# Kernel tuning notes

Measured on AMD Instinct MI355X. Metric: run time of the kernel, lower is better.

## Reference

```python
import jax, jax.numpy as jnp
import numpy as np

DILATION = 1  # module init dilation


def _pd_indexing1d(x, d, dilation):
    # x: (B, C, T) float; d: (B, 1, T) float pitch-dependent dilation factors
    B, C, T = x.shape
    dil = jnp.clip((d * dilation).astype(jnp.int32), 1)          # (B,1,T), min 1
    idx = jnp.arange(T, dtype=jnp.int32)[None, None, :]          # (1,1,T)
    idxP = jnp.abs(idx - dil) % T                                # past indices
    idxF0 = idx + dil
    # torch sets overflowed idx to -(idx % T) - 1, i.e. wraps to T - 1 - (idx % T)
    idxF = jnp.where(idxF0 >= T, T - 1 - (idxF0 % T), idxF0)     # future indices
    xP = jnp.take_along_axis(x, jnp.broadcast_to(idxP, x.shape), axis=2)
    xF = jnp.take_along_axis(x, jnp.broadcast_to(idxF, x.shape), axis=2)
    return xP, x, xF


def setup_inputs() -> dict:
    key = jax.random.key(0)
    k1, k2, k3, k4, k5, k6 = jax.random.split(key, 6)
    B, Cin, Cout, T = 8, 512, 512, 8192
    x = jax.random.normal(k1, (B, Cin, T), dtype=jnp.float32)
    d = jax.random.uniform(k2, (B, 1, T), dtype=jnp.float32)
    s = 1.0 / np.sqrt(Cin)
    W0 = jax.random.uniform(k3, (Cout, Cin), jnp.float32, -s, s)  # conv with bias
    b0 = jax.random.uniform(k4, (Cout,), jnp.float32, -s, s)
    W1 = jax.random.uniform(k5, (Cout, Cin), jnp.float32, -s, s)  # no bias
    W2 = jax.random.uniform(k6, (Cout, Cin), jnp.float32, -s, s)  # no bias
    return {"x": x, "d": d, "W0": W0, "b0": b0, "W1": W1, "W2": W2}


def reference(x, d, W0, b0, W1, W2):
    xP, xC, xF = _pd_indexing1d(x, d, DILATION)
    # three 1x1 convs (channel-mixing matmuls), summed; bias only on first conv
    out = jnp.einsum('oc,bct->bot', W0, xP) + b0[None, :, None]
    out = out + jnp.einsum('oc,bct->bot', W1, xC)
    out = out + jnp.einsum('oc,bct->bot', W2, xF)
    return out
```

## Files before the change

kernel.cpp:

```cpp
#include <hip/hip_runtime.h>

#define TT 8192
#define CIN 512
#define COUT 512
#define NB 8
#define KTOT 1536
#define NT 24

typedef __attribute__((ext_vector_type(4))) float f32x4;
typedef __attribute__((ext_vector_type(8))) short bf16x8;
typedef __attribute__((ext_vector_type(8))) unsigned short u16x8;

#define GLD16(g, l) __builtin_amdgcn_global_load_lds(                      \
    (const __attribute__((address_space(1))) void*)(g),                    \
    (__attribute__((address_space(3))) void*)(l), 16, 0, 0)

#define CFENCE() asm volatile("" ::: "memory")
#define SBAR() do { CFENCE(); __builtin_amdgcn_s_barrier(); CFENCE(); } while (0)
#define VMCNT6() asm volatile("s_waitcnt vmcnt(6)" ::: "memory")
#define VMCNT2() asm volatile("s_waitcnt vmcnt(2)" ::: "memory")
#define VMCNT0() asm volatile("s_waitcnt vmcnt(0)" ::: "memory")
#define LGKM0() asm volatile("s_waitcnt lgkmcnt(0)" ::: "memory")
#define MFMA(a_, b_, c_) __builtin_amdgcn_mfma_f32_16x16x32_bf16((a_), (b_), (c_), 0, 0, 0)

__device__ inline unsigned short f2bf(float f) {
  union { float f; unsigned int u; } v; v.f = f;
  unsigned int u = v.u;
  unsigned int r = (u + 0x7FFFu + ((u >> 16) & 1u)) >> 16;
  return (unsigned short)r;
}

__global__ void k_convert_w(const float* __restrict__ W0, const float* __restrict__ W1,
                            const float* __restrict__ W2, unsigned short* __restrict__ Wb) {
  int i = blockIdx.x * 256 + threadIdx.x;
  if (i >= COUT * CIN) return;
  const float* Ws = blockIdx.y == 0 ? W0 : (blockIdx.y == 1 ? W1 : W2);
  int o = i >> 9, c = i & 511;
  Wb[(size_t)o * KTOT + blockIdx.y * CIN + c] = f2bf(Ws[i]);
}

__global__ void k_transpose(const float* __restrict__ x, unsigned short* __restrict__ xbT,
                            int b_base) {
  int b = b_base + blockIdx.z;
  const float* xb = x + (size_t)b * CIN * TT;
  unsigned short* xo = xbT + (size_t)blockIdx.z * TT * CIN;
  __shared__ float tile[64][65];
  int t0 = blockIdx.x * 64, c0 = blockIdx.y * 64;
  int tid = threadIdx.x;
#pragma unroll
  for (int it = 0; it < 16; ++it) {
    int L = it * 256 + tid;
    int c = L >> 6, t = L & 63;
    tile[c][t] = xb[(size_t)(c0 + c) * TT + (t0 + t)];
  }
  __syncthreads();
#pragma unroll
  for (int it = 0; it < 16; ++it) {
    int L = it * 256 + tid;
    int t = L >> 6, c = L & 63;
    xo[(size_t)(t0 + t) * CIN + (c0 + c)] = f2bf(tile[c][t]);
  }
}

__global__ __launch_bounds__(512) void k_gemm256(
    const unsigned short* __restrict__ Wb, const unsigned short* __restrict__ xbT,
    const float* __restrict__ d, const float* __restrict__ bias,
    float* __restrict__ out) {
  __shared__ __align__(16) unsigned short As[2][256 * 64];
  __shared__ __align__(16) unsigned short Bs[2][256 * 64];
  const int b = blockIdx.x;
  const int t0 = (blockIdx.y >> 1) * 256;
  const int row0 = (blockIdx.y & 1) * 256;
  const unsigned short* xb = xbT + (size_t)b * TT * CIN;
  const int tid = threadIdx.x;
  const int lane = tid & 63, wid = tid >> 6;
  const int wr = wid >> 2, wc = wid & 3;
  const int l15 = lane & 15, kg = lane >> 4;

  const int srow = tid >> 3;
  const int cSrc8 = (((tid & 7) ^ ((tid >> 4) & 7))) * 8;
  int aOff[4];
  int bOff[3][4];
#pragma unroll
  for (int j = 0; j < 4; ++j) {
    int r = j * 64 + srow;
    aOff[j] = (row0 + r) * KTOT + cSrc8;
    int t = t0 + r;
    float dv = d[(size_t)b * TT + t];
    int dil = (int)dv; if (dil < 1) dil = 1;
    int p = t - dil; if (p < 0) p = -p; p &= (TT - 1);
    int f0 = t + dil;
    int f = (f0 >= TT) ? (TT - 1 - (f0 & (TT - 1))) : f0;
    bOff[0][j] = p * CIN + cSrc8;
    bOff[1][j] = t * CIN + cSrc8;
    bOff[2][j] = f * CIN + cSrc8;
  }

  const int s7 = l15 >> 1;
  const int chunk0 = (kg ^ (s7 & 3)) + (s7 & 4);
  const int dK = (l15 & 8) ? -32 : 32;
  int aRd[2][4], bRd[2][2];
#pragma unroll
  for (int mh = 0; mh < 2; ++mh)
#pragma unroll
    for (int mi = 0; mi < 4; ++mi)
      aRd[mh][mi] = (wr * 128 + mh * 64 + mi * 16 + l15) * 64 + chunk0 * 8;
#pragma unroll
  for (int nh = 0; nh < 2; ++nh)
#pragma unroll
    for (int ni = 0; ni < 2; ++ni)
      bRd[nh][ni] = (wc * 64 + nh * 32 + ni * 16 + l15) * 64 + chunk0 * 8;

#define STAGE_A_G0(tc_, buf_) do {                                            \
    GLD16(Wb + aOff[0] + (tc_) * 64, &As[buf_][0 * 4096 + wid * 512]);        \
    GLD16(Wb + aOff[2] + (tc_) * 64, &As[buf_][2 * 4096 + wid * 512]);        \
  } while (0)
#define STAGE_A_G1(tc_, buf_) do {                                            \
    GLD16(Wb + aOff[1] + (tc_) * 64, &As[buf_][1 * 4096 + wid * 512]);        \
    GLD16(Wb + aOff[3] + (tc_) * 64, &As[buf_][3 * 4096 + wid * 512]);        \
  } while (0)
#define STAGE_B4(tc_, buf_) do {                                              \
    _Pragma("unroll") for (int j = 0; j < 4; ++j)                             \
      GLD16(xb + bOff[(tc_) >> 3][j] + ((tc_) & 7) * 64,                      \
            &Bs[buf_][j * 4096 + wid * 512]);                                 \
  } while (0)

  STAGE_B4(0, 0); STAGE_A_G0(0, 0); STAGE_A_G1(0, 0);
  VMCNT0();
  SBAR();

  bf16x8 af[4][2], bf0[2][2], bf1[2][2];
  f32x4 acc[8][4] = {};

#pragma unroll 2
  for (int tc = 0; tc < NT; ++tc) {
    const int cur = tc & 1;
#pragma unroll
    for (int mi = 0; mi < 4; ++mi) {
      af[mi][0] = *(const bf16x8*)&As[cur][aRd[0][mi]];
      af[mi][1] = *(const bf16x8*)&As[cur][aRd[0][mi] + dK];
    }
#pragma unroll
    for (int ni = 0; ni < 2; ++ni) {
      bf0[ni][0] = *(const bf16x8*)&Bs[cur][bRd[0][ni]];
      bf0[ni][1] = *(const bf16x8*)&Bs[cur][bRd[0][ni] + dK];
      bf1[ni][0] = *(const bf16x8*)&Bs[cur][bRd[1][ni]];
      bf1[ni][1] = *(const bf16x8*)&Bs[cur][bRd[1][ni] + dK];
    }
    if (tc + 1 < NT) { STAGE_B4(tc + 1, cur ^ 1); STAGE_A_G0(tc + 1, cur ^ 1); }
    __builtin_amdgcn_s_setprio(1);
#pragma unroll
    for (int mi = 0; mi < 4; ++mi)
#pragma unroll
      for (int ni = 0; ni < 2; ++ni) {
        acc[mi][ni] = MFMA(af[mi][0], bf0[ni][0], acc[mi][ni]);
        acc[mi][ni] = MFMA(af[mi][1], bf0[ni][1], acc[mi][ni]);
        acc[mi][2 + ni] = MFMA(af[mi][0], bf1[ni][0], acc[mi][2 + ni]);
        acc[mi][2 + ni] = MFMA(af[mi][1], bf1[ni][1], acc[mi][2 + ni]);
      }
    __builtin_amdgcn_s_setprio(0);
    LGKM0();
    if (tc + 1 < NT) { VMCNT6(); }
    else { VMCNT0(); }
    SBAR();
#pragma unroll
    for (int mi = 0; mi < 4; ++mi) {
      af[mi][0] = *(const bf16x8*)&As[cur][aRd[1][mi]];
      af[mi][1] = *(const bf16x8*)&As[cur][aRd[1][mi] + dK];
    }
    if (tc + 1 < NT) STAGE_A_G1(tc + 1, cur ^ 1);
    __builtin_amdgcn_s_setprio(1);
#pragma unroll
    for (int mi = 0; mi < 4; ++mi)
#pragma unroll
      for (int ni = 0; ni < 2; ++ni) {
        acc[4 + mi][ni] = MFMA(af[mi][0], bf0[ni][0], acc[4 + mi][ni]);
        acc[4 + mi][ni] = MFMA(af[mi][1], bf0[ni][1], acc[4 + mi][ni]);
        acc[4 + mi][2 + ni] = MFMA(af[mi][0], bf1[ni][0], acc[4 + mi][2 + ni]);
        acc[4 + mi][2 + ni] = MFMA(af[mi][1], bf1[ni][1], acc[4 + mi][2 + ni]);
      }
    __builtin_amdgcn_s_setprio(0);
    LGKM0();
    if (tc + 1 < NT) { VMCNT2(); }
    SBAR();
  }

  float* ob = out + (size_t)b * COUT * TT;
#pragma unroll
  for (int mh = 0; mh < 2; ++mh)
#pragma unroll
    for (int mi = 0; mi < 4; ++mi) {
      int m0 = row0 + wr * 128 + mh * 64 + mi * 16 + kg * 4;
#pragma unroll
      for (int nh = 0; nh < 2; ++nh)
#pragma unroll
        for (int ni = 0; ni < 2; ++ni) {
          int t = t0 + wc * 64 + nh * 32 + ni * 16 + l15;
          f32x4 v = acc[mh * 4 + mi][nh * 2 + ni];
#pragma unroll
          for (int j = 0; j < 4; ++j)
            ob[(size_t)(m0 + j) * TT + t] = v[j] + bias[m0 + j];
        }
    }
}

__global__ __launch_bounds__(256) void k_gemm(
    const unsigned short* __restrict__ Wb, const unsigned short* __restrict__ xbT,
    const float* __restrict__ d, const float* __restrict__ bias,
    float* __restrict__ out, int b_base) {
  __shared__ __align__(16) unsigned short As[128 * 32];
  __shared__ __align__(16) unsigned short Bs[128 * 32];
  int b = b_base + blockIdx.z;
  const unsigned short* xb = xbT + (size_t)blockIdx.z * TT * CIN;
  int row0 = blockIdx.x * 128;
  int t0 = blockIdx.y * 128;
  int tid = threadIdx.x;
  int lane = tid & 63, wid = tid >> 6;
  int wr = wid >> 1, wc = wid & 1;
  int l15 = lane & 15, kg = lane >> 4;
  int rs = tid >> 2, cch = tid & 3;

  const unsigned short* aw[2];
  const unsigned short* bw[2][3];
#pragma unroll
  for (int h = 0; h < 2; ++h) {
    int r = rs + h * 64;
    int cs = cch ^ ((r >> 1) & 3);
    aw[h] = Wb + (size_t)(row0 + r) * KTOT + cs * 8;
    int t = t0 + r;
    float dv = d[(size_t)b * TT + t];
    int dil = (int)dv; if (dil < 1) dil = 1;
    int p = t - dil; if (p < 0) p = -p; p &= (TT - 1);
    int f0 = t + dil;
    int f = (f0 >= TT) ? (TT - 1 - (f0 & (TT - 1))) : f0;
    bw[h][0] = xb + (size_t)p * CIN + cs * 8;
    bw[h][1] = xb + (size_t)t * CIN + cs * 8;
    bw[h][2] = xb + (size_t)f * CIN + cs * 8;
  }
  unsigned short* aDst[2];
  unsigned short* bDst[2];
#pragma unroll
  for (int h = 0; h < 2; ++h) {
    aDst[h] = As + h * 2048 + wid * 512;
    bDst[h] = Bs + h * 2048 + wid * 512;
  }
  int aoff[4], boff[4];
#pragma unroll
  for (int mi = 0; mi < 4; ++mi) {
    int r = wr * 64 + mi * 16 + l15;
    aoff[mi] = r * 32 + (kg ^ ((r >> 1) & 3)) * 8;
  }
#pragma unroll
  for (int ni = 0; ni < 4; ++ni) {
    int r = wc * 64 + ni * 16 + l15;
    boff[ni] = r * 32 + (kg ^ ((r >> 1) & 3)) * 8;
  }
  f32x4 acc[4][4] = {};
#pragma unroll
  for (int s = 0; s < 3; ++s) {
    for (int kt = 0; kt < 16; ++kt) {
      int koff = kt * 32;
#pragma unroll
      for (int h = 0; h < 2; ++h) {
        GLD16(aw[h] + s * CIN + koff, aDst[h]);
        GLD16(bw[h][s] + koff, bDst[h]);
      }
      __syncthreads();
      bf16x8 af[4], bf[4];
#pragma unroll
      for (int mi = 0; mi < 4; ++mi) af[mi] = *(const bf16x8*)(&As[aoff[mi]]);
#pragma unroll
      for (int ni = 0; ni < 4; ++ni) bf[ni] = *(const bf16x8*)(&Bs[boff[ni]]);
#pragma unroll
      for (int mi = 0; mi < 4; ++mi)
#pragma unroll
        for (int ni = 0; ni < 4; ++ni)
          acc[mi][ni] = MFMA(af[mi], bf[ni], acc[mi][ni]);
      __syncthreads();
    }
  }
  float* ob = out + (size_t)b * COUT * TT;
#pragma unroll
  for (int mi = 0; mi < 4; ++mi) {
    int m0 = row0 + wr * 64 + mi * 16 + kg * 4;
#pragma unroll
    for (int ni = 0; ni < 4; ++ni) {
      int t = t0 + wc * 64 + ni * 16 + l15;
#pragma unroll
      for (int j = 0; j < 4; ++j) {
        ob[(size_t)(m0 + j) * TT + t] = acc[mi][ni][j] + bias[m0 + j];
      }
    }
  }
}

extern "C" void kernel_launch(void* const* d_in, const int* in_sizes, int n_in,
                              void* d_out, int out_size, void* d_ws, size_t ws_size,
                              hipStream_t stream) {
  const float* x  = (const float*)d_in[0];
  const float* d  = (const float*)d_in[1];
  const float* W0 = (const float*)d_in[2];
  const float* b0 = (const float*)d_in[3];
  const float* W1 = (const float*)d_in[4];
  const float* W2 = (const float*)d_in[5];
  float* out = (float*)d_out;

  char* ws = (char*)d_ws;
  unsigned short* Wb  = (unsigned short*)ws;
  unsigned short* xbT = (unsigned short*)(ws + (2u << 20));
  const size_t SZ_XBT1 = (size_t)TT * CIN * 2;
  const size_t NEED_FULL = (size_t)(2u << 20) + (size_t)NB * SZ_XBT1;
  const size_t NEED_MIN  = (size_t)(2u << 20) + SZ_XBT1;

  if (ws_size >= NEED_MIN) {
    k_convert_w<<<dim3(1024, 3), 256, 0, stream>>>(W0, W1, W2, Wb);
    if (ws_size >= NEED_FULL) {
      k_transpose<<<dim3(TT / 64, CIN / 64, NB), 256, 0, stream>>>(x, xbT, 0);
      k_gemm256<<<dim3(NB, (TT / 256) * (COUT / 256), 1), 512, 0, stream>>>(
          Wb, xbT, d, b0, out);
    } else {
      for (int b = 0; b < NB; ++b) {
        k_transpose<<<dim3(TT / 64, CIN / 64, 1), 256, 0, stream>>>(x, xbT, b);
        k_gemm<<<dim3(COUT / 128, TT / 128, 1), 256, 0, stream>>>(Wb, xbT, d, b0, out, b);
      }
    }
  } else {
    for (int b = 0; b < NB; ++b) {
      k_transpose<<<dim3(TT / 64, CIN / 64, 1), 256, 0, stream>>>(x, xbT, b);
      k_gemm<<<dim3(COUT / 128, TT / 128, 1), 256, 0, stream>>>(Wb, xbT, d, b0, out, b);
    }
  }
}
```

Measured before the change: 142.3 us.

## Halve K-tile to 32 and simplify gemm pipeline to single-phase double buffer

Changes the 256x256 GEMM kernel from a 64-wide K step with split A staging and partial vmcnt waits to a 32-wide K step (48 iterations), with a single stage of A and B loads per iteration and a full vmcnt(0) wait before each barrier. Shared memory per block halves, which could allow more blocks per CU, and the LDS swizzle and read pattern are simplified. In exchange there are twice as many barriers and full-drain waits, so less global-load latency is hidden behind the MFMAs.

```diff
diff --git a/kernel.cpp b/kernel.cpp
--- a/kernel.cpp
+++ b/kernel.cpp
@@ -5,11 +5,10 @@
 #define COUT 512
 #define NB 8
 #define KTOT 1536
-#define NT 24
+#define NT 48
 
 typedef __attribute__((ext_vector_type(4))) float f32x4;
 typedef __attribute__((ext_vector_type(8))) short bf16x8;
-typedef __attribute__((ext_vector_type(8))) unsigned short u16x8;
 
 #define GLD16(g, l) __builtin_amdgcn_global_load_lds(                      \
     (const __attribute__((address_space(1))) void*)(g),                    \
@@ -17,8 +16,6 @@
 
 #define CFENCE() asm volatile("" ::: "memory")
 #define SBAR() do { CFENCE(); __builtin_amdgcn_s_barrier(); CFENCE(); } while (0)
-#define VMCNT6() asm volatile("s_waitcnt vmcnt(6)" ::: "memory")
-#define VMCNT2() asm volatile("s_waitcnt vmcnt(2)" ::: "memory")
 #define VMCNT0() asm volatile("s_waitcnt vmcnt(0)" ::: "memory")
 #define LGKM0() asm volatile("s_waitcnt lgkmcnt(0)" ::: "memory")
 #define MFMA(a_, b_, c_) __builtin_amdgcn_mfma_f32_16x16x32_bf16((a_), (b_), (c_), 0, 0, 0)
@@ -66,8 +63,8 @@
     const unsigned short* __restrict__ Wb, const unsigned short* __restrict__ xbT,
     const float* __restrict__ d, const float* __restrict__ bias,
     float* __restrict__ out) {
-  __shared__ __align__(16) unsigned short As[2][256 * 64];
-  __shared__ __align__(16) unsigned short Bs[2][256 * 64];
+  __shared__ __align__(16) unsigned short As[2][256 * 32];
+  __shared__ __align__(16) unsigned short Bs[2][256 * 32];
   const int b = blockIdx.x;
   const int t0 = (blockIdx.y >> 1) * 256;
   const int row0 = (blockIdx.y & 1) * 256;
@@ -77,13 +74,13 @@
   const int wr = wid >> 2, wc = wid & 3;
   const int l15 = lane & 15, kg = lane >> 4;
 
-  const int srow = tid >> 3;
-  const int cSrc8 = (((tid & 7) ^ ((tid >> 4) & 7))) * 8;
-  int aOff[4];
-  int bOff[3][4];
-#pragma unroll
-  for (int j = 0; j < 4; ++j) {
-    int r = j * 64 + srow;
+  const int srow = tid >> 2;
+  const int cSrc8 = ((tid & 3) ^ ((tid >> 3) & 3)) * 8;
+  int aOff[2];
+  int bOffP[2], bOffC[2], bOffF[2];
+#pragma unroll
+  for (int j = 0; j < 2; ++j) {
+    int r = j * 128 + srow;
     aOff[j] = (row0 + r) * KTOT + cSrc8;
     int t = t0 + r;
     float dv = d[(size_t)b * TT + t];
@@ -91,97 +88,67 @@
     int p = t - dil; if (p < 0) p = -p; p &= (TT - 1);
     int f0 = t + dil;
     int f = (f0 >= TT) ? (TT - 1 - (f0 & (TT - 1))) : f0;
-    bOff[0][j] = p * CIN + cSrc8;
-    bOff[1][j] = t * CIN + cSrc8;
-    bOff[2][j] = f * CIN + cSrc8;
-  }
-
-  const int s7 = l15 >> 1;
-  const int chunk0 = (kg ^ (s7 & 3)) + (s7 & 4);
-  const int dK = (l15 & 8) ? -32 : 32;
-  int aRd[2][4], bRd[2][2];
+    bOffP[j] = p * CIN + cSrc8;
+    bOffC[j] = t * CIN + cSrc8;
+    bOffF[j] = f * CIN + cSrc8;
+  }
+
+  const int slot = kg ^ ((l15 >> 1) & 3);
+  int aRd[2][4], bRd[4];
 #pragma unroll
   for (int mh = 0; mh < 2; ++mh)
 #pragma unroll
     for (int mi = 0; mi < 4; ++mi)
-      aRd[mh][mi] = (wr * 128 + mh * 64 + mi * 16 + l15) * 64 + chunk0 * 8;
-#pragma unroll
-  for (int nh = 0; nh < 2; ++nh)
-#pragma unroll
-    for (int ni = 0; ni < 2; ++ni)
-      bRd[nh][ni] = (wc * 64 + nh * 32 + ni * 16 + l15) * 64 + chunk0 * 8;
-
-#define STAGE_A_G0(tc_, buf_) do {                                            \
-    GLD16(Wb + aOff[0] + (tc_) * 64, &As[buf_][0 * 4096 + wid * 512]);        \
-    GLD16(Wb + aOff[2] + (tc_) * 64, &As[buf_][2 * 4096 + wid * 512]);        \
+      aRd[mh][mi] = (wr * 128 + mh * 64 + mi * 16 + l15) * 32 + slot * 8;
+#pragma unroll
+  for (int q = 0; q < 4; ++q)
+    bRd[q] = (wc * 64 + (q >> 1) * 32 + (q & 1) * 16 + l15) * 32 + slot * 8;
+
+#define STAGE_A(tc_, buf_) do {                                               \
+    _Pragma("unroll") for (int j = 0; j < 2; ++j)                             \
+      GLD16(Wb + aOff[j] + (tc_) * 32, &As[buf_][j * 4096 + wid * 512]);      \
   } while (0)
-#define STAGE_A_G1(tc_, buf_) do {                                            \
-    GLD16(Wb + aOff[1] + (tc_) * 64, &As[buf_][1 * 4096 + wid * 512]);        \
-    GLD16(Wb + aOff[3] + (tc_) * 64, &As[buf_][3 * 4096 + wid * 512]);        \
+#define BSEL(seg_, j_) ((seg_) == 0 ? bOffP[j_] : ((seg_) == 1 ? bOffC[j_] : bOffF[j_]))
+#define STAGE_B(tc_, buf_) do {                                               \
+    int seg_ = (tc_) >> 4; int k8_ = ((tc_) & 15) * 32;                       \
+    _Pragma("unroll") for (int j = 0; j < 2; ++j)                             \
+      GLD16(xb + BSEL(seg_, j) + k8_, &Bs[buf_][j * 4096 + wid * 512]);       \
   } while (0)
-#define STAGE_B4(tc_, buf_) do {                                              \
-    _Pragma("unroll") for (int j = 0; j < 4; ++j)                             \
-      GLD16(xb + bOff[(tc_) >> 3][j] + ((tc_) & 7) * 64,                      \
-            &Bs[buf_][j * 4096 + wid * 512]);                                 \
-  } while (0)
-
-  STAGE_B4(0, 0); STAGE_A_G0(0, 0); STAGE_A_G1(0, 0);
+
+  STAGE_A(0, 0); STAGE_B(0, 0);
   VMCNT0();
   SBAR();
 
-  bf16x8 af[4][2], bf0[2][2], bf1[2][2];
+  bf16x8 af[2][4], bfr[4];
   f32x4 acc[8][4] = {};
 
 #pragma unroll 2
   for (int tc = 0; tc < NT; ++tc) {
     const int cur = tc & 1;
 #pragma unroll
-    for (int mi = 0; mi < 4; ++mi) {
-      af[mi][0] = *(const bf16x8*)&As[cur][aRd[0][mi]];
-      af[mi][1] = *(const bf16x8*)&As[cur][aRd[0][mi] + dK];
-    }
-#pragma unroll
-    for (int ni = 0; ni < 2; ++ni) {
-      bf0[ni][0] = *(const bf16x8*)&Bs[cur][bRd[0][ni]];
-      bf0[ni][1] = *(const bf16x8*)&Bs[cur][bRd[0][ni] + dK];
-      bf1[ni][0] = *(const bf16x8*)&Bs[cur][bRd[1][ni]];
-      bf1[ni][1] = *(const bf16x8*)&Bs[cur][bRd[1][ni] + dK];
-    }
-    if (tc + 1 < NT) { STAGE_B4(tc + 1, cur ^ 1); STAGE_A_G0(tc + 1, cur ^ 1); }
+    for (int q = 0; q < 4; ++q) bfr[q] = *(const bf16x8*)&Bs[cur][bRd[q]];
+#pragma unroll
+    for (int mh = 0; mh < 2; ++mh)
+#pragma unroll
+      for (int mi = 0; mi < 4; ++mi)
+        af[mh][mi] = *(const bf16x8*)&As[cur][aRd[mh][mi]];
+    if (tc + 1 < NT) { STAGE_A(tc + 1, cur ^ 1); STAGE_B(tc + 1, cur ^ 1); }
     __builtin_amdgcn_s_setprio(1);
 #pragma unroll
     for (int mi = 0; mi < 4; ++mi)
 #pragma unroll
-      for (int ni = 0; ni < 2; ++ni) {
-        acc[mi][ni] = MFMA(af[mi][0], bf0[ni][0], acc[mi][ni]);
-        acc[mi][ni] = MFMA(af[mi][1], bf0[ni][1], acc[mi][ni]);
-        acc[mi][2 + ni] = MFMA(af[mi][0], bf1[ni][0], acc[mi][2 + ni]);
-        acc[mi][2 + ni] = MFMA(af[mi][1], bf1[ni][1], acc[mi][2 + ni]);
-      }
+      for (int q = 0; q < 4; ++q)
+        acc[mi][q] = MFMA(af[0][mi], bfr[q], acc[mi][q]);
+    __builtin_amdgcn_s_setprio(0);
+    __builtin_amdgcn_s_setprio(1);
+#pragma unroll
+    for (int mi = 0; mi < 4; ++mi)
+#pragma unroll
+      for (int q = 0; q < 4; ++q)
+        acc[4 + mi][q] = MFMA(af[1][mi], bfr[q], acc[4 + mi][q]);
     __builtin_amdgcn_s_setprio(0);
     LGKM0();
-    if (tc + 1 < NT) { VMCNT6(); }
-    else { VMCNT0(); }
-    SBAR();
-#pragma unroll
-    for (int mi = 0; mi < 4; ++mi) {
-      af[mi][0] = *(const bf16x8*)&As[cur][aRd[1][mi]];
-      af[mi][1] = *(const bf16x8*)&As[cur][aRd[1][mi] + dK];
-    }
-    if (tc + 1 < NT) STAGE_A_G1(tc + 1, cur ^ 1);
-    __builtin_amdgcn_s_setprio(1);
-#pragma unroll
-    for (int mi = 0; mi < 4; ++mi)
-#pragma unroll
-      for (int ni = 0; ni < 2; ++ni) {
-        acc[4 + mi][ni] = MFMA(af[mi][0], bf0[ni][0], acc[4 + mi][ni]);
-        acc[4 + mi][ni] = MFMA(af[mi][1], bf0[ni][1], acc[4 + mi][ni]);
-        acc[4 + mi][2 + ni] = MFMA(af[mi][0], bf1[ni][0], acc[4 + mi][2 + ni]);
-        acc[4 + mi][2 + ni] = MFMA(af[mi][1], bf1[ni][1], acc[4 + mi][2 + ni]);
-      }
-    __builtin_amdgcn_s_setprio(0);
-    LGKM0();
-    if (tc + 1 < NT) { VMCNT2(); }
+    if (tc + 1 < NT) VMCNT0();
     SBAR();
   }
 
@@ -192,15 +159,13 @@
     for (int mi = 0; mi < 4; ++mi) {
       int m0 = row0 + wr * 128 + mh * 64 + mi * 16 + kg * 4;
 #pragma unroll
-      for (int nh = 0; nh < 2; ++nh)
-#pragma unroll
-        for (int ni = 0; ni < 2; ++ni) {
-          int t = t0 + wc * 64 + nh * 32 + ni * 16 + l15;
-          f32x4 v = acc[mh * 4 + mi][nh * 2 + ni];
-#pragma unroll
-          for (int j = 0; j < 4; ++j)
-            ob[(size_t)(m0 + j) * TT + t] = v[j] + bias[m0 + j];
-        }
+      for (int q = 0; q < 4; ++q) {
+        int t = t0 + wc * 64 + (q >> 1) * 32 + (q & 1) * 16 + l15;
+        f32x4 v = acc[mh * 4 + mi][q];
+#pragma unroll
+        for (int j = 0; j < 4; ++j)
+          ob[(size_t)(m0 + j) * TT + t] = v[j] + bias[m0 + j];
+      }
     }
 }
 
```

After: 159.7 us. 12.2% more time.
